# Performance work log

Hardware: AMD Instinct MI355X
Metric: run time of the kernel (lower is better)

The kernel has to match this reference:

```python
import jax, jax.numpy as jnp
import numpy as np

T, B = 128, 256          # frames, batch (free dims)
C_IN = 201               # in_features
KD = 3                   # keypoint_dimensionality
NK = C_IN // KD          # 67 keypoints = attention seq len
E = 8                    # d_pose_embed
H = 2                    # heads
DH = E // H              # head dim = 4
L = 12                   # encoder layers
FF = 2 * E               # 16
OUT = 128                # output_size
EPS = 1e-5


def setup_inputs() -> dict:
    key = jax.random.key(0)
    ks = jax.random.split(key, 12)
    s = 0.1
    return {
        "pose_clip": jax.random.normal(ks[0], (T, B, C_IN), jnp.float32),
        "embed_w": jax.random.normal(ks[1], (E, KD), jnp.float32) * s,
        "embed_b": jax.random.normal(ks[2], (E,), jnp.float32) * s,
        "in_proj_w": jax.random.normal(ks[3], (L, 3 * E, E), jnp.float32) * s,
        "in_proj_b": jax.random.normal(ks[4], (L, 3 * E), jnp.float32) * s,
        "attn_out_w": jax.random.normal(ks[5], (L, E, E), jnp.float32) * s,
        "attn_out_b": jax.random.normal(ks[6], (L, E), jnp.float32) * s,
        "ff1_w": jax.random.normal(ks[7], (L, FF, E), jnp.float32) * s,
        "ff1_b": jax.random.normal(ks[8], (L, FF), jnp.float32) * s,
        "ff2_w": jax.random.normal(ks[9], (L, E, FF), jnp.float32) * s,
        "ff2_b": jax.random.normal(ks[10], (L, E), jnp.float32) * s,
        "ln1_g": jnp.ones((L, E), jnp.float32),
        "ln1_b": jnp.zeros((L, E), jnp.float32),
        "ln2_g": jnp.ones((L, E), jnp.float32),
        "ln2_b": jnp.zeros((L, E), jnp.float32),
        "out_w": jax.random.normal(ks[11], (OUT, NK * E), jnp.float32) * s,
        "out_b": jnp.zeros((OUT,), jnp.float32),
    }


def _ln(x, g, b):
    m = jnp.mean(x, axis=-1, keepdims=True)
    v = jnp.mean(jnp.square(x - m), axis=-1, keepdims=True)
    return (x - m) * jax.lax.rsqrt(v + EPS) * g + b


def _encoder(x, layer_params):
    # x: [S, N, E]; post-LN TransformerEncoderLayer, relu activation, no dropout (eval)
    def step(h, p):
        ipw, ipb, aow, aob, f1w, f1b, f2w, f2b, g1, b1, g2, b2 = p
        S, N, _ = h.shape
        qkv = h @ ipw.T + ipb                      # [S, N, 3E]
        q, k, v = jnp.split(qkv, 3, axis=-1)
        q = q.reshape(S, N, H, DH)
        k = k.reshape(S, N, H, DH)
        v = v.reshape(S, N, H, DH)
        scores = jnp.einsum('snhd,tnhd->nhst', q, k) / np.sqrt(DH).astype(h.dtype)
        attn = jax.nn.softmax(scores, axis=-1)
        o = jnp.einsum('nhst,tnhd->snhd', attn, v).reshape(S, N, E)
        o = o @ aow.T + aob
        h = _ln(h + o, g1, b1)
        ff = jax.nn.relu(h @ f1w.T + f1b) @ f2w.T + f2b
        h = _ln(h + ff, g2, b2)
        return h, None
    x, _ = jax.lax.scan(step, x, layer_params)
    return x


def reference(pose_clip, embed_w, embed_b, in_proj_w, in_proj_b, attn_out_w,
              attn_out_b, ff1_w, ff1_b, ff2_w, ff2_b, ln1_g, ln1_b, ln2_g,
              ln2_b, out_w, out_b):
    t, b, c = pose_clip.shape
    nk = c // KD
    # [t,b,c] -> [t*b, nk, 3] -> [nk, t*b, 3]  (seq=keypoints, batch=t*b)
    x = pose_clip.reshape(t * b, nk, KD).transpose(1, 0, 2)
    x = x @ embed_w.T + embed_b                    # [nk, t*b, E]
    layer_params = (in_proj_w, in_proj_b, attn_out_w, attn_out_b,
                    ff1_w, ff1_b, ff2_w, ff2_b, ln1_g, ln1_b, ln2_g, ln2_b)
    x = _encoder(x, layer_params)
    x = x.transpose(1, 0, 2).reshape(t, b, nk * E)  # [t, b, 536]
    return jnp.tanh(x @ out_w.T + out_b)            # [t, b, 128]
```

## Files before the change

kernel.cpp:

```cpp
#include <hip/hip_runtime.h>
#include <math.h>

#define NTOT 32768
#define CIN  201
#define S    67
#define E    8
#define H    2
#define L    12
#define FF   16
#define OUTC 128
#define KF   536
#define EPB  7
#define LPE  34
#define THREADS 256
#define NPAIR 34

typedef float v2f __attribute__((ext_vector_type(2)));
typedef __fp16 h2  __attribute__((ext_vector_type(2)));

#if __has_builtin(__builtin_amdgcn_exp2f)
#define EXP2F(x) __builtin_amdgcn_exp2f(x)
#else
#define EXP2F(x) exp2f(x)
#endif
#if __has_builtin(__builtin_amdgcn_rcpf)
#define RCPF(x) __builtin_amdgcn_rcpf(x)
#else
#define RCPF(x) (1.0f/(x))
#endif
#if __has_builtin(__builtin_amdgcn_rsqf)
#define RSQF(x) __builtin_amdgcn_rsqf(x)
#else
#define RSQF(x) rsqrtf(x)
#endif

#if __has_builtin(__builtin_amdgcn_cvt_pkrtz)
__device__ __forceinline__ h2 cvh(float a, float b) {
    return __builtin_amdgcn_cvt_pkrtz(a, b);
}
#else
__device__ __forceinline__ h2 cvh(float a, float b) {
    h2 r; r.x = (__fp16)a; r.y = (__fp16)b; return r;
}
#endif
__device__ __forceinline__ float pkf(float a, float b) {
    return __builtin_bit_cast(float, cvh(a, b));
}
__device__ __forceinline__ h2 bch(float f) { return __builtin_bit_cast(h2, f); }

#if __has_builtin(__builtin_amdgcn_fdot2)
#define FDOT2(a, b, c) __builtin_amdgcn_fdot2((a), (b), (c), false)
#else
#define FDOT2(a, b, c) ((float)(a).x*(float)(b).x + (float)(a).y*(float)(b).y + (c))
#endif

#define QSCALE 0.7213475204444817f

__device__ __forceinline__ v2f sp(float x) { return (v2f){x, x}; }

__device__ __forceinline__ void ln8p(v2f* x, const float* __restrict__ gg,
                                     const float* __restrict__ bb) {
    v2f m = {0.f, 0.f};
    #pragma unroll
    for (int e = 0; e < E; ++e) m += x[e];
    m *= 0.125f;
    v2f v = {0.f, 0.f};
    #pragma unroll
    for (int e = 0; e < E; ++e) { v2f d = x[e] - m; v += d * d; }
    v *= 0.125f;
    v2f rs;
    rs.x = RSQF(v.x + 1e-5f);
    rs.y = RSQF(v.y + 1e-5f);
    #pragma unroll
    for (int e = 0; e < E; ++e) x[e] = (x[e] - m) * rs * sp(gg[e]) + sp(bb[e]);
}

__global__ __launch_bounds__(THREADS, 8)
void enc_kernel(const float* __restrict__ pose,
                const float* __restrict__ ew,  const float* __restrict__ ebias,
                const float* __restrict__ ipw, const float* __restrict__ ipb,
                const float* __restrict__ aow, const float* __restrict__ aob,
                const float* __restrict__ f1w, const float* __restrict__ f1b,
                const float* __restrict__ f2w, const float* __restrict__ f2b,
                const float* __restrict__ g1,  const float* __restrict__ b1,
                const float* __restrict__ g2,  const float* __restrict__ b2,
                float* __restrict__ xf)
{
    __shared__ float4 Kh[EPB * H][NPAIR];
    __shared__ float4 Vh[EPB * H][NPAIR];

    const int lid = threadIdx.x;
    const int g   = lid / LPE;
    const int j   = lid - g * LPE;
    const int n   = blockIdx.x * EPB + g;
    const bool active = (g < EPB) && (n < NTOT);
    const bool pad = (j == LPE - 1);
    const int r0 = 2 * j;

    v2f xr[E];
    if (active) {
        const float* p0 = pose + (size_t)n * CIN + 3 * r0;
        const float* p1 = pad ? p0 : (p0 + 3);
        v2f c0 = {p0[0], p1[0]};
        v2f c1 = {p0[1], p1[1]};
        v2f c2 = {p0[2], p1[2]};
        #pragma unroll
        for (int e = 0; e < E; ++e)
            xr[e] = sp(ebias[e]) + c0 * sp(ew[e*3+0]) + c1 * sp(ew[e*3+1])
                                 + c2 * sp(ew[e*3+2]);
    }

    #pragma unroll 1
    for (int l = 0; l < L; ++l) {
        const float* W  = ipw + l * 192;
        const float* Bq = ipb + l * 24;

        h2 qh[8];
        if (active) {
            v2f kv[16];
            #pragma unroll
            for (int jo = 0; jo < 16; ++jo) {
                v2f a = sp(Bq[8 + jo]);
                #pragma unroll
                for (int e = 0; e < E; ++e) a += xr[e] * sp(W[(8+jo)*8 + e]);
                kv[jo] = a;
            }
            if (pad) {
                #pragma unroll
                for (int c = 0; c < 16; ++c) kv[c].y = 0.f;
            }
            #pragma unroll
            for (int h = 0; h < H; ++h) {
                const int gh = g*2 + h;
                Kh[gh][j] = make_float4(
                    pkf(kv[4*h+0].x, kv[4*h+1].x),
                    pkf(kv[4*h+2].x, kv[4*h+3].x),
                    pkf(kv[4*h+0].y, kv[4*h+1].y),
                    pkf(kv[4*h+2].y, kv[4*h+3].y));
                Vh[gh][j] = make_float4(
                    pkf(kv[8+4*h+0].x, kv[8+4*h+0].y),
                    pkf(kv[8+4*h+1].x, kv[8+4*h+1].y),
                    pkf(kv[8+4*h+2].x, kv[8+4*h+2].y),
                    pkf(kv[8+4*h+3].x, kv[8+4*h+3].y));
            }
            #pragma unroll
            for (int h = 0; h < H; ++h) {
                v2f q[4];
                #pragma unroll
                for (int c = 0; c < 4; ++c) {
                    v2f a = sp(Bq[4*h + c]);
                    #pragma unroll
                    for (int e = 0; e < E; ++e) a += xr[e] * sp(W[(4*h+c)*8 + e]);
                    q[c] = a * QSCALE;
                }
                qh[4*h+0] = cvh(q[0].x, q[1].x);
                qh[4*h+1] = cvh(q[2].x, q[3].x);
                qh[4*h+2] = cvh(q[0].y, q[1].y);
                qh[4*h+3] = cvh(q[2].y, q[3].y);
            }
        }
        __syncthreads();

        if (active) {
            const h2 one2 = cvh(1.0f, 1.0f);
            v2f os[E];
            #pragma unroll
            for (int h = 0; h < H; ++h) {
                const int gh = g*2 + h;
                const float4* pK = Kh[gh];
                const float4* pV = Vh[gh];
                const h2 q01_0 = qh[4*h+0], q23_0 = qh[4*h+1];
                const h2 q01_1 = qh[4*h+2], q23_1 = qh[4*h+3];
                float ls0 = 0.f, ls1 = 0.f;
                float oc00=0.f, oc01=0.f, oc02=0.f, oc03=0.f;
                float oc10=0.f, oc11=0.f, oc12=0.f, oc13=0.f;
                #pragma unroll
                for (int i = 0; i < NPAIR; ++i) {
                    float4 kk = pK[i];
                    float4 vv = pV[i];
                    h2 ka = bch(kk.x), kb = bch(kk.y);
                    h2 kc = bch(kk.z), kd = bch(kk.w);
                    float s00 = FDOT2(q01_0, ka, FDOT2(q23_0, kb, 0.f));
                    float s01 = FDOT2(q01_0, kc, FDOT2(q23_0, kd, 0.f));
                    float s10 = FDOT2(q01_1, ka, FDOT2(q23_1, kb, 0.f));
                    float s11 = FDOT2(q01_1, kc, FDOT2(q23_1, kd, 0.f));
                    float e00 = EXP2F(s00), e01 = EXP2F(s01);
                    float e10 = EXP2F(s10), e11 = EXP2F(s11);
                    h2 ep0 = cvh(e00, e01);
                    h2 ep1 = cvh(e10, e11);
                    ls0 = FDOT2(ep0, one2, ls0);
                    ls1 = FDOT2(ep1, one2, ls1);
                    h2 v0 = bch(vv.x), v1 = bch(vv.y);
                    h2 v2 = bch(vv.z), v3 = bch(vv.w);
                    oc00 = FDOT2(ep0, v0, oc00); oc01 = FDOT2(ep0, v1, oc01);
                    oc02 = FDOT2(ep0, v2, oc02); oc03 = FDOT2(ep0, v3, oc03);
                    oc10 = FDOT2(ep1, v0, oc10); oc11 = FDOT2(ep1, v1, oc11);
                    oc12 = FDOT2(ep1, v2, oc12); oc13 = FDOT2(ep1, v3, oc13);
                }
                float l0 = ls0 - 1.0f;
                float l1 = ls1 - 1.0f;
                float i0 = RCPF(l0), i1 = RCPF(l1);
                os[4*h+0] = (v2f){oc00*i0, oc10*i1};
                os[4*h+1] = (v2f){oc01*i0, oc11*i1};
                os[4*h+2] = (v2f){oc02*i0, oc12*i1};
                os[4*h+3] = (v2f){oc03*i0, oc13*i1};
            }

            {
                const float* WA = aow + l*64;
                const float* BA = aob + l*8;
                #pragma unroll
                for (int e = 0; e < E; ++e) {
                    v2f a = sp(BA[e]);
                    #pragma unroll
                    for (int e2 = 0; e2 < E; ++e2) a += os[e2] * sp(WA[e*8 + e2]);
                    xr[e] += a;
                }
            }
            ln8p(xr, g1 + l*E, b1 + l*E);

            {
                const float* W1 = f1w + l*128;
                const float* B1 = f1b + l*16;
                const float* W2 = f2w + l*128;
                const float* B2 = f2b + l*8;
                v2f t1[FF];
                #pragma unroll
                for (int f = 0; f < FF; ++f) {
                    v2f a = sp(B1[f]);
                    #pragma unroll
                    for (int e = 0; e < E; ++e) a += xr[e] * sp(W1[f*8 + e]);
                    a.x = fmaxf(a.x, 0.f);
                    a.y = fmaxf(a.y, 0.f);
                    t1[f] = a;
                }
                #pragma unroll
                for (int e = 0; e < E; ++e) {
                    v2f a = sp(B2[e]);
                    #pragma unroll
                    for (int f = 0; f < FF; ++f) a += t1[f] * sp(W2[e*16 + f]);
                    xr[e] += a;
                }
            }
            ln8p(xr, g2 + l*E, b2 + l*E);
        }
        __syncthreads();
    }

    if (active) {
        float* dst = xf + (size_t)n * KF + r0 * E;
        *(float4*)(dst + 0) = make_float4(xr[0].x, xr[1].x, xr[2].x, xr[3].x);
        *(float4*)(dst + 4) = make_float4(xr[4].x, xr[5].x, xr[6].x, xr[7].x);
        if (!pad) {
            *(float4*)(dst + 8)  = make_float4(xr[0].y, xr[1].y, xr[2].y, xr[3].y);
            *(float4*)(dst + 12) = make_float4(xr[4].y, xr[5].y, xr[6].y, xr[7].y);
        }
    }
}

__global__ void tr_kernel(const float* __restrict__ ow, float* __restrict__ wt)
{
    int i = blockIdx.x * 256 + threadIdx.x;
    if (i < OUTC * KF) {
        int c = i / KF, k = i - c * KF;
        wt[k * OUTC + c] = ow[i];
    }
}

__global__ __launch_bounds__(256, 4)
void out_kernel(const float* __restrict__ xf, const float* __restrict__ wt,
                const float* __restrict__ ob, float* __restrict__ out)
{
    __shared__ float Xs[32][68];
    const int lid = threadIdx.x;
    const int tx  = lid & 31;
    const int ty  = lid >> 5;
    const int n0  = blockIdx.x * 32;

    float acc[4][4] = {};

    #pragma unroll 1
    for (int kc = 0; kc < 9; ++kc) {
        const int kb = kc * 64;
        const int kw = (kc < 8) ? 64 : 24;
        __syncthreads();
        const int nvec = 32 * (kw >> 2);
        for (int i = lid; i < nvec; i += 256) {
            int r = i / (kw >> 2), kq = i - r * (kw >> 2);
            *(float4*)&Xs[r][kq*4] =
                *(const float4*)&xf[(size_t)(n0 + r) * KF + kb + kq*4];
        }
        __syncthreads();
        #pragma unroll 4
        for (int k = 0; k < kw; ++k) {
            float4 w4 = *(const float4*)&wt[(size_t)(kb + k) * OUTC + tx*4];
            #pragma unroll
            for (int i = 0; i < 4; ++i) {
                float x = Xs[ty*4 + i][k];
                acc[i][0] += x*w4.x; acc[i][1] += x*w4.y;
                acc[i][2] += x*w4.z; acc[i][3] += x*w4.w;
            }
        }
    }

    const float4 bb = *(const float4*)&ob[tx*4];
    #pragma unroll
    for (int i = 0; i < 4; ++i) {
        int r = n0 + ty*4 + i;
        float4 v;
        v.x = tanhf(acc[i][0] + bb.x);
        v.y = tanhf(acc[i][1] + bb.y);
        v.z = tanhf(acc[i][2] + bb.z);
        v.w = tanhf(acc[i][3] + bb.w);
        *(float4*)(out + (size_t)r * OUTC + tx*4) = v;
    }
}

extern "C" void kernel_launch(void* const* d_in, const int* in_sizes, int n_in,
                              void* d_out, int out_size, void* d_ws, size_t ws_size,
                              hipStream_t stream) {
    (void)in_sizes; (void)n_in; (void)out_size; (void)ws_size;
    const float* pose = (const float*)d_in[0];
    const float* ew   = (const float*)d_in[1];
    const float* eb   = (const float*)d_in[2];
    const float* ipw  = (const float*)d_in[3];
    const float* ipb  = (const float*)d_in[4];
    const float* aow  = (const float*)d_in[5];
    const float* aob  = (const float*)d_in[6];
    const float* f1w  = (const float*)d_in[7];
    const float* f1b  = (const float*)d_in[8];
    const float* f2w  = (const float*)d_in[9];
    const float* f2b  = (const float*)d_in[10];
    const float* g1   = (const float*)d_in[11];
    const float* b1   = (const float*)d_in[12];
    const float* g2   = (const float*)d_in[13];
    const float* b2   = (const float*)d_in[14];
    const float* ow   = (const float*)d_in[15];
    const float* ob   = (const float*)d_in[16];

    float* xf = (float*)d_ws;
    float* wt = xf + (size_t)NTOT * KF;

    const int grid1 = (NTOT + EPB - 1) / EPB;
    enc_kernel<<<grid1, THREADS, 0, stream>>>(pose, ew, eb, ipw, ipb, aow, aob,
                                              f1w, f1b, f2w, f2b, g1, b1, g2, b2, xf);
    tr_kernel<<<(OUTC*KF + 255)/256, 256, 0, stream>>>(ow, wt);
    out_kernel<<<NTOT / 32, 256, 0, stream>>>(xf, wt, ob, (float*)d_out);
}
```

Baseline: 1.372 ms.

## Pre-pack layer weights to fp16 pairs and use packed dot2 for all projections

Adds a pack kernel that converts each layer's QKV, attention-out and FFN weights into fp16 pairs, with the Q scale folded in, and stores them with the biases in one contiguous per-layer block. The encoder converts activations to fp16 pairs and computes every projection with fdot2 instead of fp32 FMAs. This roughly halves the arithmetic instruction count and the number of scalar weight loads. In exchange it lowers projection precision to fp16 and relaxes launch bounds from 8 to 6 blocks per CU. The packed buffer shares workspace with the transposed output weights, which tr_kernel overwrites afterwards; that ordering is fine on a single stream.

```diff
diff --git a/kernel.cpp b/kernel.cpp
--- a/kernel.cpp
+++ b/kernel.cpp
@@ -3,7 +3,6 @@
 
 #define NTOT 32768
 #define CIN  201
-#define S    67
 #define E    8
 #define H    2
 #define L    12
@@ -14,6 +13,7 @@
 #define LPE  34
 #define THREADS 256
 #define NPAIR 34
+#define PWL  320
 
 typedef float v2f __attribute__((ext_vector_type(2)));
 typedef __fp16 h2  __attribute__((ext_vector_type(2)));
@@ -58,6 +58,15 @@
 
 __device__ __forceinline__ v2f sp(float x) { return (v2f){x, x}; }
 
+__device__ __forceinline__ float dot4h(const h2* x, const float* __restrict__ w,
+                                       float acc) {
+    acc = FDOT2(x[0], bch(w[0]), acc);
+    acc = FDOT2(x[1], bch(w[1]), acc);
+    acc = FDOT2(x[2], bch(w[2]), acc);
+    acc = FDOT2(x[3], bch(w[3]), acc);
+    return acc;
+}
+
 __device__ __forceinline__ void ln8p(v2f* x, const float* __restrict__ gg,
                                      const float* __restrict__ bb) {
     v2f m = {0.f, 0.f};
@@ -75,13 +84,43 @@
     for (int e = 0; e < E; ++e) x[e] = (x[e] - m) * rs * sp(gg[e]) + sp(bb[e]);
 }
 
-__global__ __launch_bounds__(THREADS, 8)
+__global__ void pack_kernel(const float* __restrict__ ipw, const float* __restrict__ ipb,
+                            const float* __restrict__ aow, const float* __restrict__ aob,
+                            const float* __restrict__ f1w, const float* __restrict__ f1b,
+                            const float* __restrict__ f2w, const float* __restrict__ f2b,
+                            float* __restrict__ wpk)
+{
+    const int l = blockIdx.x, t = threadIdx.x;
+    float* D = wpk + l * PWL;
+    if (t < 96) {
+        int jo = t >> 2, p = t & 3;
+        float s = (jo < 8) ? QSCALE : 1.0f;
+        D[t] = pkf(ipw[l*192 + jo*8 + 2*p] * s, ipw[l*192 + jo*8 + 2*p + 1] * s);
+    } else if (t < 128) {
+        int i = t - 96, e = i >> 2, p = i & 3;
+        D[t] = pkf(aow[l*64 + e*8 + 2*p], aow[l*64 + e*8 + 2*p + 1]);
+    } else if (t < 192) {
+        int i = t - 128, f = i >> 2, p = i & 3;
+        D[t] = pkf(f1w[l*128 + f*8 + 2*p], f1w[l*128 + f*8 + 2*p + 1]);
+    } else if (t < 256) {
+        int i = t - 192, e = i >> 3, p = i & 7;
+        D[t] = pkf(f2w[l*128 + e*16 + 2*p], f2w[l*128 + e*16 + 2*p + 1]);
+    } else if (t < 280) {
+        int c = t - 256;
+        D[t] = ipb[l*24 + c] * ((c < 8) ? QSCALE : 1.0f);
+    } else if (t < 288) {
+        D[t] = aob[l*8 + (t - 280)];
+    } else if (t < 304) {
+        D[t] = f1b[l*16 + (t - 288)];
+    } else if (t < 312) {
+        D[t] = f2b[l*8 + (t - 304)];
+    }
+}
+
+__global__ __launch_bounds__(THREADS, 6)
 void enc_kernel(const float* __restrict__ pose,
                 const float* __restrict__ ew,  const float* __restrict__ ebias,
-                const float* __restrict__ ipw, const float* __restrict__ ipb,
-                const float* __restrict__ aow, const float* __restrict__ aob,
-                const float* __restrict__ f1w, const float* __restrict__ f1b,
-                const float* __restrict__ f2w, const float* __restrict__ f2b,
+                const float* __restrict__ wpk,
                 const float* __restrict__ g1,  const float* __restrict__ b1,
                 const float* __restrict__ g2,  const float* __restrict__ b2,
                 float* __restrict__ xf)
@@ -112,51 +151,57 @@
 
     #pragma unroll 1
     for (int l = 0; l < L; ++l) {
-        const float* W  = ipw + l * 192;
-        const float* Bq = ipb + l * 24;
+        const float* PW = wpk + l * PWL;
 
         h2 qh[8];
         if (active) {
-            v2f kv[16];
+            h2 xh0[4], xh1[4];
             #pragma unroll
-            for (int jo = 0; jo < 16; ++jo) {
-                v2f a = sp(Bq[8 + jo]);
-                #pragma unroll
-                for (int e = 0; e < E; ++e) a += xr[e] * sp(W[(8+jo)*8 + e]);
-                kv[jo] = a;
-            }
-            if (pad) {
-                #pragma unroll
-                for (int c = 0; c < 16; ++c) kv[c].y = 0.f;
+            for (int p = 0; p < 4; ++p) {
+                xh0[p] = cvh(xr[2*p].x, xr[2*p+1].x);
+                xh1[p] = cvh(xr[2*p].y, xr[2*p+1].y);
             }
             #pragma unroll
             for (int h = 0; h < H; ++h) {
                 const int gh = g*2 + h;
-                Kh[gh][j] = make_float4(
-                    pkf(kv[4*h+0].x, kv[4*h+1].x),
-                    pkf(kv[4*h+2].x, kv[4*h+3].x),
-                    pkf(kv[4*h+0].y, kv[4*h+1].y),
-                    pkf(kv[4*h+2].y, kv[4*h+3].y));
-                Vh[gh][j] = make_float4(
-                    pkf(kv[8+4*h+0].x, kv[8+4*h+0].y),
-                    pkf(kv[8+4*h+1].x, kv[8+4*h+1].y),
-                    pkf(kv[8+4*h+2].x, kv[8+4*h+2].y),
-                    pkf(kv[8+4*h+3].x, kv[8+4*h+3].y));
+                float kr0[4], kr1[4];
+                #pragma unroll
+                for (int c = 0; c < 4; ++c) {
+                    const int jo = 8 + 4*h + c;
+                    const float* wr = PW + jo*4;
+                    const float b = PW[256 + jo];
+                    kr0[c] = dot4h(xh0, wr, b);
+                    kr1[c] = pad ? 0.f : dot4h(xh1, wr, b);
+                }
+                Kh[gh][j] = make_float4(pkf(kr0[0], kr0[1]), pkf(kr0[2], kr0[3]),
+                                        pkf(kr1[0], kr1[1]), pkf(kr1[2], kr1[3]));
+                float vr0[4], vr1[4];
+                #pragma unroll
+                for (int c = 0; c < 4; ++c) {
+                    const int jo = 16 + 4*h + c;
+                    const float* wr = PW + jo*4;
+                    const float b = PW[256 + jo];
+                    vr0[c] = dot4h(xh0, wr, b);
+                    vr1[c] = pad ? 0.f : dot4h(xh1, wr, b);
+                }
+                Vh[gh][j] = make_float4(pkf(vr0[0], vr1[0]), pkf(vr0[1], vr1[1]),
+                                        pkf(vr0[2], vr1[2]), pkf(vr0[3], vr1[3]));
             }
             #pragma unroll
             for (int h = 0; h < H; ++h) {
-                v2f q[4];
+                float q0[4], q1[4];
                 #pragma unroll
                 for (int c = 0; c < 4; ++c) {
-                    v2f a = sp(Bq[4*h + c]);
-                    #pragma unroll
-                    for (int e = 0; e < E; ++e) a += xr[e] * sp(W[(4*h+c)*8 + e]);
-                    q[c] = a * QSCALE;
-                }
-                qh[4*h+0] = cvh(q[0].x, q[1].x);
-                qh[4*h+1] = cvh(q[2].x, q[3].x);
-                qh[4*h+2] = cvh(q[0].y, q[1].y);
-                qh[4*h+3] = cvh(q[2].y, q[3].y);
+                    const int jo = 4*h + c;
+                    const float* wr = PW + jo*4;
+                    const float b = PW[256 + jo];
+                    q0[c] = dot4h(xh0, wr, b);
+                    q1[c] = dot4h(xh1, wr, b);
+                }
+                qh[4*h+0] = cvh(q0[0], q0[1]);
+                qh[4*h+1] = cvh(q0[2], q0[3]);
+                qh[4*h+2] = cvh(q1[0], q1[1]);
+                qh[4*h+3] = cvh(q1[2], q1[3]);
             }
         }
         __syncthreads();
@@ -207,39 +252,54 @@
             }
 
             {
-                const float* WA = aow + l*64;
-                const float* BA = aob + l*8;
+                h2 oh0[4], oh1[4];
+                #pragma unroll
+                for (int p = 0; p < 4; ++p) {
+                    oh0[p] = cvh(os[2*p].x, os[2*p+1].x);
+                    oh1[p] = cvh(os[2*p].y, os[2*p+1].y);
+                }
                 #pragma unroll
                 for (int e = 0; e < E; ++e) {
-                    v2f a = sp(BA[e]);
+                    const float* wr = PW + 96 + e*4;
+                    const float b = PW[280 + e];
+                    float a0 = dot4h(oh0, wr, b);
+                    float a1 = dot4h(oh1, wr, b);
+                    xr[e] += (v2f){a0, a1};
+                }
+            }
+            ln8p(xr, g1 + l*E, b1 + l*E);
+
+            {
+                h2 xh0[4], xh1[4];
+                #pragma unroll
+                for (int p = 0; p < 4; ++p) {
+                    xh0[p] = cvh(xr[2*p].x, xr[2*p+1].x);
+                    xh1[p] = cvh(xr[2*p].y, xr[2*p+1].y);
+                }
+                h2 th0[8], th1[8];
+                #pragma unroll
+                for (int p = 0; p < 8; ++p) {
+                    const float* wa = PW + 128 + (2*p)*4;
+                    const float* wb = PW + 128 + (2*p+1)*4;
+                    const float ba = PW[288 + 2*p], bb = PW[288 + 2*p + 1];
+                    float t00 = fmaxf(dot4h(xh0, wa, ba), 0.f);
+                    float t01 = fmaxf(dot4h(xh0, wb, bb), 0.f);
+                    float t10 = fmaxf(dot4h(xh1, wa, ba), 0.f);
+                    float t11 = fmaxf(dot4h(xh1, wb, bb), 0.f);
+                    th0[p] = cvh(t00, t01);
+                    th1[p] = cvh(t10, t11);
+                }
+                #pragma unroll
+                for (int e = 0; e < E; ++e) {
+                    const float* wr = PW + 192 + e*8;
+                    const float b = PW[304 + e];
+                    float a0 = b, a1 = b;
                     #pragma unroll
-                    for (int e2 = 0; e2 < E; ++e2) a += os[e2] * sp(WA[e*8 + e2]);
-                    xr[e] += a;
-                }
-            }
-            ln8p(xr, g1 + l*E, b1 + l*E);
-
-            {
-                const float* W1 = f1w + l*128;
-                const float* B1 = f1b + l*16;
-                const float* W2 = f2w + l*128;
-                const float* B2 = f2b + l*8;
-                v2f t1[FF];
-                #pragma unroll
-                for (int f = 0; f < FF; ++f) {
-                    v2f a = sp(B1[f]);
-                    #pragma unroll
-                    for (int e = 0; e < E; ++e) a += xr[e] * sp(W1[f*8 + e]);
-                    a.x = fmaxf(a.x, 0.f);
-                    a.y = fmaxf(a.y, 0.f);
-                    t1[f] = a;
-                }
-                #pragma unroll
-                for (int e = 0; e < E; ++e) {
-                    v2f a = sp(B2[e]);
-                    #pragma unroll
-                    for (int f = 0; f < FF; ++f) a += t1[f] * sp(W2[e*16 + f]);
-                    xr[e] += a;
+                    for (int p = 0; p < 8; ++p) {
+                        a0 = FDOT2(th0[p], bch(wr[p]), a0);
+                        a1 = FDOT2(th1[p], bch(wr[p]), a1);
+                    }
+                    xr[e] += (v2f){a0, a1};
                 }
             }
             ln8p(xr, g2 + l*E, b2 + l*E);
@@ -338,12 +398,15 @@
     const float* ow   = (const float*)d_in[15];
     const float* ob   = (const float*)d_in[16];
 
-    float* xf = (float*)d_ws;
-    float* wt = xf + (size_t)NTOT * KF;
+    float* xf  = (float*)d_ws;
+    float* wt  = xf + (size_t)NTOT * KF;
+    float* wpk = wt;
+
+    pack_kernel<<<L, 320, 0, stream>>>(ipw, ipb, aow, aob, f1w, f1b, f2w, f2b, wpk);
 
     const int grid1 = (NTOT + EPB - 1) / EPB;
-    enc_kernel<<<grid1, THREADS, 0, stream>>>(pose, ew, eb, ipw, ipb, aow, aob,
-                                              f1w, f1b, f2w, f2b, g1, b1, g2, b2, xf);
+    enc_kernel<<<grid1, THREADS, 0, stream>>>(pose, ew, eb, wpk,
+                                              g1, b1, g2, b2, xf);
     tr_kernel<<<(OUTC*KF + 255)/256, 256, 0, stream>>>(ow, wt);
     out_kernel<<<NTOT / 32, 256, 0, stream>>>(xf, wt, ob, (float*)d_out);
 }
```

After: 1.380 ms. Within noise of the previous version (+0.5%).
